# Kernel optimization log

Hardware: AMD Instinct MI355X
Metric: run time of the kernel (lower is better)

The kernel has to match this reference:

```python
import jax, jax.numpy as jnp
import numpy as np
from jax import lax

POOL = 4  # hp['gcn_pool_size']


def sparsemax(z):
    # sparsemax along last axis (Martins & Astudillo 2016), matches tfa.activations.sparsemax
    n = z.shape[-1]
    z_sorted = jnp.flip(jnp.sort(z, axis=-1), axis=-1)          # descending
    k = jnp.arange(1, n + 1, dtype=z.dtype)
    zcum = jnp.cumsum(z_sorted, axis=-1)
    support = (1.0 + k * z_sorted) > zcum                        # [.., n] bool
    k_sel = jnp.sum(support, axis=-1, keepdims=True)             # int, >= 1
    tau = (jnp.take_along_axis(zcum, k_sel - 1, axis=-1) - 1.0) / k_sel.astype(z.dtype)
    return jnp.maximum(z - tau, 0.0)


def gcn_layer(x, W):
    # x: [B, T, E]
    T = x.shape[1]
    # einsum('Bte,bte->tBb') then mean over t == contract over t,e and divide by T
    adj = jnp.einsum('Bte,bte->Bb', x, x) / T                    # [B, B]
    adj = sparsemax(adj)                                         # row-wise sparsemax
    m = adj[:, :, None, None] * x[None]                          # [B, b, T, E] outer product
    # MaxPool2D((POOL,1), stride 1, 'same') on [batch=B, H=b, W=T, C=E]: pool over neighbor axis b
    m = lax.reduce_window(m, -jnp.inf, lax.max,
                          (1, POOL, 1, 1), (1, 1, 1, 1), 'SAME')
    agg = jnp.sum(m, axis=1)                                     # [B, T, E]
    return jax.nn.relu(agg @ W)                                  # [B, T, rel_dim]


def setup_inputs() -> dict:
    key = jax.random.key(0)
    k0, k1, k2, k3 = jax.random.split(key, 4)
    B, T, E = 64, 256, 64
    rel_dim, n_stack = 4, 8
    x = jax.random.normal(k0, (B, T, E), dtype=jnp.float32)
    W0 = jax.random.normal(k1, (E, rel_dim), dtype=jnp.float32) * 0.1
    W1 = jax.random.normal(k2, (rel_dim, rel_dim), dtype=jnp.float32) * 0.1
    Wp = jax.random.normal(k3, (rel_dim, n_stack), dtype=jnp.float32) * 0.1
    return {"x": x, "W0": W0, "W1": W1, "Wp": Wp}


def reference(x, W0, W1, Wp):
    x = gcn_layer(x, W0)           # layer 0: E -> rel_dim
    x = gcn_layer(x, W1)           # layer 1: rel_dim -> rel_dim
    pooled = jnp.mean(x, axis=1)   # [B, rel_dim], mean over T
    return jax.nn.softmax(pooled @ Wp, axis=-1)  # [B, n_stack]
```

## Files before the change

### kernel.cpp

```cpp
#include <hip/hip_runtime.h>
#include <math.h>

__device__ __forceinline__ float4 f4max(float4 a, float4 b) {
    return make_float4(fmaxf(a.x, b.x), fmaxf(a.y, b.y), fmaxf(a.z, b.z), fmaxf(a.w, b.w));
}
__device__ __forceinline__ float4 f4scale(float s, float4 v) {
    return make_float4(s * v.x, s * v.y, s * v.z, s * v.w);
}
__device__ __forceinline__ float4 f4add(float4 a, float4 b) {
    return make_float4(a.x + b.x, a.y + b.y, a.z + b.z, a.w + b.w);
}
__device__ __forceinline__ float4 f4fma(float a, float4 b, float4 c) {
    return make_float4(fmaf(a, b.x, c.x), fmaf(a, b.y, c.y), fmaf(a, b.z, c.z), fmaf(a, b.w, c.w));
}
__device__ __forceinline__ float4 f4fma4(float4 a, float4 b, float4 c) {
    return make_float4(fmaf(a.x, b.x, c.x), fmaf(a.y, b.y, c.y),
                       fmaf(a.z, b.z, c.z), fmaf(a.w, b.w, c.w));
}

__device__ __forceinline__ void store_f4_llc(float* p, float4 v) {
    __hip_atomic_store(p + 0, v.x, __ATOMIC_RELAXED, __HIP_MEMORY_SCOPE_AGENT);
    __hip_atomic_store(p + 1, v.y, __ATOMIC_RELAXED, __HIP_MEMORY_SCOPE_AGENT);
    __hip_atomic_store(p + 2, v.z, __ATOMIC_RELAXED, __HIP_MEMORY_SCOPE_AGENT);
    __hip_atomic_store(p + 3, v.w, __ATOMIC_RELAXED, __HIP_MEMORY_SCOPE_AGENT);
}

__device__ __forceinline__ float wave_sparsemax(float z, int lane) {
    float v = z;
    for (int k = 2; k <= 64; k <<= 1) {
        bool desc = (lane & k) == 0;
        for (int j = k >> 1; j > 0; j >>= 1) {
            float other = __shfl_xor(v, j, 64);
            bool lower = (lane & j) == 0;
            float mn = fminf(v, other), mx = fmaxf(v, other);
            v = (desc ^ lower) ? mn : mx;
        }
    }
    float c = v;
    for (int d = 1; d < 64; d <<= 1) {
        float n = __shfl_up(c, d, 64);
        if (lane >= d) c += n;
    }
    bool sup = (1.0f + (float)(lane + 1) * v) > c;
    int ksel = __popcll(__ballot(sup));
    float zk = __shfl(c, ksel - 1, 64);
    float tau = (zk - 1.0f) / (float)ksel;
    return fmaxf(z - tau, 0.f);
}

__device__ unsigned g_grp[16 * 64];
__device__ unsigned g_glb;
__device__ unsigned g_gen1;
__device__ unsigned g_gen2;

__device__ __forceinline__ void sync_point(int bx, unsigned snap, unsigned* genp,
                                           bool wait) {
    __syncthreads();
    if (threadIdx.x == 0) {
        unsigned a = __hip_atomic_fetch_add(&g_grp[(bx & 15) << 6], 1u,
                                            __ATOMIC_RELAXED, __HIP_MEMORY_SCOPE_AGENT);
        if ((a & 15u) == 15u) {
            unsigned ga = __hip_atomic_fetch_add(&g_glb, 1u, __ATOMIC_RELAXED,
                                                 __HIP_MEMORY_SCOPE_AGENT);
            if ((ga & 15u) == 15u)
                __hip_atomic_fetch_add(genp, 1u, __ATOMIC_RELAXED,
                                       __HIP_MEMORY_SCOPE_AGENT);
        }
        if (wait) {
            while (__hip_atomic_load(genp, __ATOMIC_RELAXED,
                                     __HIP_MEMORY_SCOPE_AGENT) == snap)
                __builtin_amdgcn_s_sleep(1);
            __builtin_amdgcn_fence(__ATOMIC_ACQUIRE, "agent");
        }
    }
    if (wait) __syncthreads();
}

__global__ __launch_bounds__(256)
void fused_gcn(const float* __restrict__ x, const float* __restrict__ W0,
               const float* __restrict__ W1, const float* __restrict__ Wp,
               float* __restrict__ P, float* __restrict__ h0,
               float* __restrict__ out) {
    __shared__ float xsT[64][68];
    __shared__ float pstg[4][4][64];
    __shared__ float psm_s[4][64];
    __shared__ __align__(16) float row[4 * 260];
    __shared__ float part[256];
    __shared__ float psmD[64];
    __shared__ float red[16];

    int tid = threadIdx.x;
    int bx = blockIdx.x;
    int lane = tid & 63;

    unsigned snap1 = 0, snap2 = 0;
    if (tid == 0) {
        snap1 = __hip_atomic_load(&g_gen1, __ATOMIC_RELAXED, __HIP_MEMORY_SCOPE_AGENT);
        snap2 = __hip_atomic_load(&g_gen2, __ATOMIC_RELAXED, __HIP_MEMORY_SCOPE_AGENT);
    }

    {
        int k0 = bx * 64;
#pragma unroll
        for (int it = 0; it < 4; ++it) {
            int f = it * 256 + tid;
            int i = f >> 4, k4 = (f & 15) * 4;
            float4 v = *(const float4*)(x + (size_t)i * 16384 + k0 + k4);
            xsT[k4 + 0][i] = v.x; xsT[k4 + 1][i] = v.y;
            xsT[k4 + 2][i] = v.z; xsT[k4 + 3][i] = v.w;
        }
        __syncthreads();
        int ti = (tid >> 4) * 4, tj = (tid & 15) * 4;
        float4 a0 = make_float4(0, 0, 0, 0), a1 = a0, a2 = a0, a3 = a0;
#pragma unroll 8
        for (int k = 0; k < 64; ++k) {
            float4 a = *(const float4*)&xsT[k][ti];
            float4 b = *(const float4*)&xsT[k][tj];
            a0 = f4fma(a.x, b, a0); a1 = f4fma(a.y, b, a1);
            a2 = f4fma(a.z, b, a2); a3 = f4fma(a.w, b, a3);
        }
        float* basep = P + ((size_t)bx << 12);
        store_f4_llc(basep + (ti + 0) * 64 + tj, a0);
        store_f4_llc(basep + (ti + 1) * 64 + tj, a1);
        store_f4_llc(basep + (ti + 2) * 64 + tj, a2);
        store_f4_llc(basep + (ti + 3) * 64 + tj, a3);
    }
    sync_point(bx, snap1, &g_gen1, true);

    {
        int w4 = tid >> 6;
        int Bc = (bx & 15) * 4;
        int rowi = Bc + w4;
        int sub = (tid & 63) >> 4;
        int c16 = tid & 15;
        const float* pb = P + (size_t)rowi * 64 + c16 * 4;
        float4 g = make_float4(0, 0, 0, 0);
        int cbase = sub * 64;
#pragma unroll 8
        for (int i = 0; i < 64; ++i)
            g = f4add(g, *(const float4*)(pb + ((size_t)(cbase + i) << 12)));
        *(float4*)&pstg[w4][sub][c16 * 4] = g;
        __syncthreads();
        {
            float z = (((pstg[w4][0][lane] + pstg[w4][1][lane])
                        + pstg[w4][2][lane]) + pstg[w4][3][lane]) * (1.0f / 256.0f);
            psm_s[w4][lane] = wave_sparsemax(z, lane);
        }
        __syncthreads();
    }

    {
        int t0 = (bx >> 4) * 16;
        int Bc = (bx & 15) * 4;
        int w = __builtin_amdgcn_readfirstlane(tid >> 6);
        int tq = lane >> 4, eq = lane & 15;
        int t = t0 + (w << 2) + tq;
        float4 w0r0 = *(const float4*)(W0 + (eq * 4 + 0) * 4);
        float4 w0r1 = *(const float4*)(W0 + (eq * 4 + 1) * 4);
        float4 w0r2 = *(const float4*)(W0 + (eq * 4 + 2) * 4);
        float4 w0r3 = *(const float4*)(W0 + (eq * 4 + 3) * 4);
        const float4* xg = (const float4*)(x + ((size_t)t * 64) + eq * 4);
        float4 qm1[4], qb[4], vt[4], acc[4];
        float4 xA = xg[0];
        float4 xB = xg[4096];
#pragma unroll
        for (int h = 0; h < 4; ++h) {
            float4 v = f4scale(psm_s[h][0], xA);
            vt[h] = f4scale(psm_s[h][1], xB);
            qm1[h] = v;
            qb[h] = f4max(v, vt[h]);
            acc[h] = make_float4(0, 0, 0, 0);
        }
#pragma unroll 4
        for (int bl = 0; bl < 62; ++bl) {
            float4 xn = xg[(size_t)(bl + 2) * 4096];
#pragma unroll
            for (int h = 0; h < 4; ++h) {
                float4 vn = f4scale(psm_s[h][bl + 2], xn);
                float4 q1 = f4max(vt[h], vn);
                acc[h] = f4add(acc[h], f4max(qm1[h], q1));
                qm1[h] = qb[h]; qb[h] = q1; vt[h] = vn;
            }
        }
#pragma unroll
        for (int h = 0; h < 4; ++h) {
            acc[h] = f4add(acc[h], f4max(qm1[h], vt[h]));
            acc[h] = f4add(acc[h], qb[h]);
            float4 a = acc[h];
            float4 hh = f4fma(a.x, w0r0, f4fma(a.y, w0r1,
                       f4fma(a.z, w0r2, f4scale(a.w, w0r3))));
            for (int m = 1; m <= 8; m <<= 1) {
                hh.x += __shfl_xor(hh.x, m, 64);
                hh.y += __shfl_xor(hh.y, m, 64);
                hh.z += __shfl_xor(hh.z, m, 64);
                hh.w += __shfl_xor(hh.w, m, 64);
            }
            if (eq == 0) {
                int B = Bc + h;
                float4 r = make_float4(fmaxf(hh.x, 0.f), fmaxf(hh.y, 0.f),
                                       fmaxf(hh.z, 0.f), fmaxf(hh.w, 0.f));
                store_f4_llc(h0 + (size_t)(B * 256 + t) * 4, r);
            }
        }
    }
    sync_point(bx, snap2, &g_gen2, bx < 64);

    if (bx < 64) {
        int bid = bx;
        {
            int q = tid >> 6, s2 = (tid & 63) * 4;
            *(float4*)(row + q * 260 + s2) = *(const float4*)(h0 + (size_t)bid * 1024 + tid * 4);
        }
        __syncthreads();
        {
            int j = tid >> 2, q = tid & 3;
            const float4* hj = (const float4*)(h0 + (size_t)j * 1024 + q * 256);
            const float4* ri = (const float4*)(row + q * 260);
            float4 s4 = make_float4(0, 0, 0, 0);
#pragma unroll 8
            for (int kk = 0; kk < 64; ++kk) s4 = f4fma4(ri[kk], hj[kk], s4);
            part[tid] = s4.x + s4.y + s4.z + s4.w;
        }
        __syncthreads();
        if (tid < 64) {
            float z = (part[lane * 4] + part[lane * 4 + 1] + part[lane * 4 + 2]
                       + part[lane * 4 + 3]) * (1.0f / 256.0f);
            psmD[lane] = wave_sparsemax(z, lane);
        }
        __syncthreads();
        int w = __builtin_amdgcn_readfirstlane(tid >> 6);
        int rc = lane & 3;
        float psum = 0.f;
#pragma unroll
        for (int gg = 0; gg < 4; ++gg) {
            int tbase = w * 64 + gg * 16;
            const float* xb = h0 + (size_t)tbase * 4 + lane;
            float v0 = psmD[0] * xb[0];
            float v1 = psmD[1] * xb[1024];
            float qm1s = v0, qbs = fmaxf(v0, v1), vts = v1, accs = 0.f;
#pragma unroll 8
            for (int bl = 0; bl < 62; ++bl) {
                float vn = psmD[bl + 2] * xb[(size_t)(bl + 2) * 1024];
                float q1 = fmaxf(vts, vn);
                accs += fmaxf(qm1s, q1);
                qm1s = qbs; qbs = q1; vts = vn;
            }
            accs += fmaxf(qm1s, vts);
            accs += qbs;
            int base = lane & ~3;
            float b0 = __shfl(accs, base + 0, 64);
            float b1 = __shfl(accs, base + 1, 64);
            float b2 = __shfl(accs, base + 2, 64);
            float b3 = __shfl(accs, base + 3, 64);
            float h = b0 * W1[rc] + b1 * W1[4 + rc] + b2 * W1[8 + rc] + b3 * W1[12 + rc];
            psum += fmaxf(h, 0.f);
        }
        for (int m = 4; m <= 32; m <<= 1) psum += __shfl_xor(psum, m, 64);
        if (lane < 4) red[w * 4 + lane] = psum;
        __syncthreads();
        if (tid < 64) {
            float pooled = 0.f;
            if (lane < 4)
                pooled = (red[lane] + red[4 + lane] + red[8 + lane] + red[12 + lane])
                         * (1.0f / 256.0f);
            float q0 = __shfl(pooled, 0, 64), q1 = __shfl(pooled, 1, 64);
            float q2 = __shfl(pooled, 2, 64), q3 = __shfl(pooled, 3, 64);
            float logit = -INFINITY;
            if (lane < 8)
                logit = q0 * Wp[lane] + q1 * Wp[8 + lane]
                      + q2 * Wp[16 + lane] + q3 * Wp[24 + lane];
            float mx = logit;
            for (int m = 4; m >= 1; m >>= 1) mx = fmaxf(mx, __shfl_xor(mx, m, 8));
            float e = (lane < 8) ? __expf(logit - mx) : 0.f;
            float s = e;
            for (int m = 4; m >= 1; m >>= 1) s += __shfl_xor(s, m, 8);
            if (lane < 8) out[bid * 8 + lane] = e / s;
        }
    }
}

extern "C" void kernel_launch(void* const* d_in, const int* in_sizes, int n_in,
                              void* d_out, int out_size, void* d_ws, size_t ws_size,
                              hipStream_t stream) {
    const float* x  = (const float*)d_in[0];
    const float* W0 = (const float*)d_in[1];
    const float* W1 = (const float*)d_in[2];
    const float* Wp = (const float*)d_in[3];
    float* out = (float*)d_out;

    char* ws = (char*)d_ws;
    float* P  = (float*)ws;
    float* h0 = (float*)(ws + (4u << 20));

    fused_gcn<<<256, 256, 0, stream>>>(x, W0, W1, Wp, P, h0, out);
}
```

Before: 116.5 us.

## Deduplicate cross-block partial reduction via extra grid barrier and staging buffer

Replaces the per-block redundant reduction of Gram-matrix partials (each of 16 blocks per row group re-reading all 256 partial chunks) with a one-time distributed reduction into a new P2 staging buffer. This is followed by an additional grid-wide sync before blocks read their reduced rows. It aims to cut L2/global read traffic by a factor of 16, at the cost of a third grid barrier and a reduction phase where only 4 lanes per wave are active.

```diff
diff --git a/kernel.cpp b/kernel.cpp
--- a/kernel.cpp
+++ b/kernel.cpp
@@ -51,6 +51,7 @@
 __device__ unsigned g_grp[16 * 64];
 __device__ unsigned g_glb;
 __device__ unsigned g_gen1;
+__device__ unsigned g_gen3;
 __device__ unsigned g_gen2;
 
 __device__ __forceinline__ void sync_point(int bx, unsigned snap, unsigned* genp,
@@ -79,8 +80,8 @@
 __global__ __launch_bounds__(256)
 void fused_gcn(const float* __restrict__ x, const float* __restrict__ W0,
                const float* __restrict__ W1, const float* __restrict__ Wp,
-               float* __restrict__ P, float* __restrict__ h0,
-               float* __restrict__ out) {
+               float* __restrict__ P, float* __restrict__ P2,
+               float* __restrict__ h0, float* __restrict__ out) {
     __shared__ float xsT[64][68];
     __shared__ float pstg[4][4][64];
     __shared__ float psm_s[4][64];
@@ -93,10 +94,11 @@
     int bx = blockIdx.x;
     int lane = tid & 63;
 
-    unsigned snap1 = 0, snap2 = 0;
+    unsigned snap1 = 0, snap2 = 0, snap3 = 0;
     if (tid == 0) {
         snap1 = __hip_atomic_load(&g_gen1, __ATOMIC_RELAXED, __HIP_MEMORY_SCOPE_AGENT);
-        snap2 = __hip_atomic_load(&g_gen2, __ATOMIC_RELAXED, __HIP_MEMORY_SCOPE_AGENT);
+        snap2 = __hip_atomic_load(&g_gen3, __ATOMIC_RELAXED, __HIP_MEMORY_SCOPE_AGENT);
+        snap3 = __hip_atomic_load(&g_gen2, __ATOMIC_RELAXED, __HIP_MEMORY_SCOPE_AGENT);
     }
 
     {
@@ -129,17 +131,30 @@
 
     {
         int w4 = tid >> 6;
+        int l = tid & 63;
+        if (l < 4) {
+            int cid = (bx << 4) + (w4 << 2) + l;
+            int i = cid >> 6;
+            int q = (cid >> 2) & 15;
+            int s = cid & 3;
+            const float* pb = P + (size_t)i * 64 + q * 4;
+            int cbase = s << 6;
+            float4 g = make_float4(0, 0, 0, 0);
+#pragma unroll 8
+            for (int c = 0; c < 64; ++c)
+                g = f4add(g, *(const float4*)(pb + ((size_t)(cbase + c) << 12)));
+            store_f4_llc(P2 + (((size_t)(i * 16 + q) * 4 + s) << 2), g);
+        }
+    }
+    sync_point(bx, snap2, &g_gen3, true);
+
+    {
+        int w4 = tid >> 6;
         int Bc = (bx & 15) * 4;
         int rowi = Bc + w4;
-        int sub = (tid & 63) >> 4;
-        int c16 = tid & 15;
-        const float* pb = P + (size_t)rowi * 64 + c16 * 4;
-        float4 g = make_float4(0, 0, 0, 0);
-        int cbase = sub * 64;
-#pragma unroll 8
-        for (int i = 0; i < 64; ++i)
-            g = f4add(g, *(const float4*)(pb + ((size_t)(cbase + i) << 12)));
-        *(float4*)&pstg[w4][sub][c16 * 4] = g;
+        int q = lane >> 2, s = lane & 3;
+        float4 v = *(const float4*)(P2 + (((size_t)(rowi * 16 + q) * 4 + s) << 2));
+        *(float4*)&pstg[w4][s][q * 4] = v;
         __syncthreads();
         {
             float z = (((pstg[w4][0][lane] + pstg[w4][1][lane])
@@ -203,7 +218,7 @@
             }
         }
     }
-    sync_point(bx, snap2, &g_gen2, bx < 64);
+    sync_point(bx, snap3, &g_gen2, bx < 64);
 
     if (bx < 64) {
         int bid = bx;
@@ -291,6 +306,7 @@
     char* ws = (char*)d_ws;
     float* P  = (float*)ws;
     float* h0 = (float*)(ws + (4u << 20));
-
-    fused_gcn<<<256, 256, 0, stream>>>(x, W0, W1, Wp, P, h0, out);
-}
+    float* P2 = (float*)(ws + (4u << 20) + 262144u);
+
+    fused_gcn<<<256, 256, 0, stream>>>(x, W0, W1, Wp, P, P2, h0, out);
+}
```

Result: slower. 121.9 us (+4.7%).

## Double block size to 512 threads and split per-wave work across more waves

Applied to the files above, without the earlier changes.

Launches 512 threads per block instead of 256. Each phase redistributes its work: the Gram tile computes 2 rows per thread, the aggregation phase gives each wave 2 batch rows instead of 4, and the final layer-1 phase packs two batch items per block using 32 blocks. The aim is to shorten the serial chain per wave and raise latency hiding in the memory-bound streaming loops, at the cost of more barrier participants and idle waves during the sparsemax reduction.

```diff
diff --git a/kernel.cpp b/kernel.cpp
--- a/kernel.cpp
+++ b/kernel.cpp
@@ -76,7 +76,7 @@
     if (wait) __syncthreads();
 }
 
-__global__ __launch_bounds__(256)
+__global__ __launch_bounds__(512)
 void fused_gcn(const float* __restrict__ x, const float* __restrict__ W0,
                const float* __restrict__ W1, const float* __restrict__ Wp,
                float* __restrict__ P, float* __restrict__ h0,
@@ -84,10 +84,10 @@
     __shared__ float xsT[64][68];
     __shared__ float pstg[4][4][64];
     __shared__ float psm_s[4][64];
-    __shared__ __align__(16) float row[4 * 260];
-    __shared__ float part[256];
-    __shared__ float psmD[64];
-    __shared__ float red[16];
+    __shared__ __align__(16) float rowD[2][4 * 260];
+    __shared__ float part[2][256];
+    __shared__ float psmD[2][64];
+    __shared__ float redD[2][16];
 
     int tid = threadIdx.x;
     int bx = blockIdx.x;
@@ -102,57 +102,59 @@
     {
         int k0 = bx * 64;
 #pragma unroll
-        for (int it = 0; it < 4; ++it) {
-            int f = it * 256 + tid;
+        for (int it = 0; it < 2; ++it) {
+            int f = it * 512 + tid;
             int i = f >> 4, k4 = (f & 15) * 4;
             float4 v = *(const float4*)(x + (size_t)i * 16384 + k0 + k4);
             xsT[k4 + 0][i] = v.x; xsT[k4 + 1][i] = v.y;
             xsT[k4 + 2][i] = v.z; xsT[k4 + 3][i] = v.w;
         }
         __syncthreads();
-        int ti = (tid >> 4) * 4, tj = (tid & 15) * 4;
-        float4 a0 = make_float4(0, 0, 0, 0), a1 = a0, a2 = a0, a3 = a0;
+        int ti = (tid >> 4) * 2, tj = (tid & 15) * 4;
+        float4 a0 = make_float4(0, 0, 0, 0), a1 = a0;
 #pragma unroll 8
         for (int k = 0; k < 64; ++k) {
-            float4 a = *(const float4*)&xsT[k][ti];
+            float ax = xsT[k][ti], ay = xsT[k][ti + 1];
             float4 b = *(const float4*)&xsT[k][tj];
-            a0 = f4fma(a.x, b, a0); a1 = f4fma(a.y, b, a1);
-            a2 = f4fma(a.z, b, a2); a3 = f4fma(a.w, b, a3);
+            a0 = f4fma(ax, b, a0); a1 = f4fma(ay, b, a1);
         }
         float* basep = P + ((size_t)bx << 12);
         store_f4_llc(basep + (ti + 0) * 64 + tj, a0);
         store_f4_llc(basep + (ti + 1) * 64 + tj, a1);
-        store_f4_llc(basep + (ti + 2) * 64 + tj, a2);
-        store_f4_llc(basep + (ti + 3) * 64 + tj, a3);
     }
     sync_point(bx, snap1, &g_gen1, true);
 
     {
-        int w4 = tid >> 6;
+        int w8 = tid >> 6;
         int Bc = (bx & 15) * 4;
-        int rowi = Bc + w4;
-        int sub = (tid & 63) >> 4;
-        int c16 = tid & 15;
-        const float* pb = P + (size_t)rowi * 64 + c16 * 4;
-        float4 g = make_float4(0, 0, 0, 0);
-        int cbase = sub * 64;
+        if (w8 < 4) {
+            int rowi = Bc + w8;
+            int sub = lane >> 4;
+            int c16 = lane & 15;
+            const float* pb = P + (size_t)rowi * 64 + c16 * 4;
+            int cbase = sub * 64;
+            float4 g = make_float4(0, 0, 0, 0);
 #pragma unroll 8
-        for (int i = 0; i < 64; ++i)
-            g = f4add(g, *(const float4*)(pb + ((size_t)(cbase + i) << 12)));
-        *(float4*)&pstg[w4][sub][c16 * 4] = g;
-        __syncthreads();
-        {
-            float z = (((pstg[w4][0][lane] + pstg[w4][1][lane])
-                        + pstg[w4][2][lane]) + pstg[w4][3][lane]) * (1.0f / 256.0f);
-            psm_s[w4][lane] = wave_sparsemax(z, lane);
+            for (int c = 0; c < 64; ++c)
+                g = f4add(g, *(const float4*)(pb + ((size_t)(cbase + c) << 12)));
+            *(float4*)&pstg[w8][sub][c16 * 4] = g;
+        }
+        __syncthreads();
+        if (w8 < 4) {
+            float z = (((pstg[w8][0][lane] + pstg[w8][1][lane])
+                        + pstg[w8][2][lane]) + pstg[w8][3][lane]) * (1.0f / 256.0f);
+            psm_s[w8][lane] = wave_sparsemax(z, lane);
         }
         __syncthreads();
     }
 
     {
         int t0 = (bx >> 4) * 16;
-        int Bc = (bx & 15) * 4;
-        int w = __builtin_amdgcn_readfirstlane(tid >> 6);
+        int BcBase = (bx & 15) * 4;
+        int w8 = __builtin_amdgcn_readfirstlane(tid >> 6);
+        int vb = w8 >> 2;
+        int w = w8 & 3;
+        int hb = vb * 2;
         int tq = lane >> 4, eq = lane & 15;
         int t = t0 + (w << 2) + tq;
         float4 w0r0 = *(const float4*)(W0 + (eq * 4 + 0) * 4);
@@ -160,13 +162,13 @@
         float4 w0r2 = *(const float4*)(W0 + (eq * 4 + 2) * 4);
         float4 w0r3 = *(const float4*)(W0 + (eq * 4 + 3) * 4);
         const float4* xg = (const float4*)(x + ((size_t)t * 64) + eq * 4);
-        float4 qm1[4], qb[4], vt[4], acc[4];
+        float4 qm1[2], qb[2], vt[2], acc[2];
         float4 xA = xg[0];
         float4 xB = xg[4096];
 #pragma unroll
-        for (int h = 0; h < 4; ++h) {
-            float4 v = f4scale(psm_s[h][0], xA);
-            vt[h] = f4scale(psm_s[h][1], xB);
+        for (int h = 0; h < 2; ++h) {
+            float4 v = f4scale(psm_s[hb + h][0], xA);
+            vt[h] = f4scale(psm_s[hb + h][1], xB);
             qm1[h] = v;
             qb[h] = f4max(v, vt[h]);
             acc[h] = make_float4(0, 0, 0, 0);
@@ -175,15 +177,15 @@
         for (int bl = 0; bl < 62; ++bl) {
             float4 xn = xg[(size_t)(bl + 2) * 4096];
 #pragma unroll
-            for (int h = 0; h < 4; ++h) {
-                float4 vn = f4scale(psm_s[h][bl + 2], xn);
+            for (int h = 0; h < 2; ++h) {
+                float4 vn = f4scale(psm_s[hb + h][bl + 2], xn);
                 float4 q1 = f4max(vt[h], vn);
                 acc[h] = f4add(acc[h], f4max(qm1[h], q1));
                 qm1[h] = qb[h]; qb[h] = q1; vt[h] = vn;
             }
         }
 #pragma unroll
-        for (int h = 0; h < 4; ++h) {
+        for (int h = 0; h < 2; ++h) {
             acc[h] = f4add(acc[h], f4max(qm1[h], vt[h]));
             acc[h] = f4add(acc[h], qb[h]);
             float4 a = acc[h];
@@ -196,51 +198,55 @@
                 hh.w += __shfl_xor(hh.w, m, 64);
             }
             if (eq == 0) {
-                int B = Bc + h;
+                int B = BcBase + hb + h;
                 float4 r = make_float4(fmaxf(hh.x, 0.f), fmaxf(hh.y, 0.f),
                                        fmaxf(hh.z, 0.f), fmaxf(hh.w, 0.f));
                 store_f4_llc(h0 + (size_t)(B * 256 + t) * 4, r);
             }
         }
     }
-    sync_point(bx, snap2, &g_gen2, bx < 64);
-
-    if (bx < 64) {
-        int bid = bx;
+    sync_point(bx, snap2, &g_gen2, bx < 32);
+
+    if (bx < 32) {
+        int vb = tid >> 8;
+        int ttid = tid & 255;
+        int bid = bx * 2 + vb;
         {
-            int q = tid >> 6, s2 = (tid & 63) * 4;
-            *(float4*)(row + q * 260 + s2) = *(const float4*)(h0 + (size_t)bid * 1024 + tid * 4);
+            int q = ttid >> 6, s2 = lane * 4;
+            *(float4*)(rowD[vb] + q * 260 + s2) =
+                *(const float4*)(h0 + (size_t)bid * 1024 + ttid * 4);
         }
         __syncthreads();
         {
-            int j = tid >> 2, q = tid & 3;
+            int j = ttid >> 2, q = ttid & 3;
             const float4* hj = (const float4*)(h0 + (size_t)j * 1024 + q * 256);
-            const float4* ri = (const float4*)(row + q * 260);
+            const float4* ri = (const float4*)(rowD[vb] + q * 260);
             float4 s4 = make_float4(0, 0, 0, 0);
 #pragma unroll 8
             for (int kk = 0; kk < 64; ++kk) s4 = f4fma4(ri[kk], hj[kk], s4);
-            part[tid] = s4.x + s4.y + s4.z + s4.w;
-        }
-        __syncthreads();
-        if (tid < 64) {
-            float z = (part[lane * 4] + part[lane * 4 + 1] + part[lane * 4 + 2]
-                       + part[lane * 4 + 3]) * (1.0f / 256.0f);
-            psmD[lane] = wave_sparsemax(z, lane);
-        }
-        __syncthreads();
-        int w = __builtin_amdgcn_readfirstlane(tid >> 6);
+            part[vb][ttid] = s4.x + s4.y + s4.z + s4.w;
+        }
+        __syncthreads();
+        if (ttid < 64) {
+            float z = (part[vb][lane * 4] + part[vb][lane * 4 + 1]
+                       + part[vb][lane * 4 + 2] + part[vb][lane * 4 + 3])
+                      * (1.0f / 256.0f);
+            psmD[vb][lane] = wave_sparsemax(z, lane);
+        }
+        __syncthreads();
+        int w = __builtin_amdgcn_readfirstlane((tid >> 6) & 3);
         int rc = lane & 3;
         float psum = 0.f;
 #pragma unroll
         for (int gg = 0; gg < 4; ++gg) {
             int tbase = w * 64 + gg * 16;
             const float* xb = h0 + (size_t)tbase * 4 + lane;
-            float v0 = psmD[0] * xb[0];
-            float v1 = psmD[1] * xb[1024];
+            float v0 = psmD[vb][0] * xb[0];
+            float v1 = psmD[vb][1] * xb[1024];
             float qm1s = v0, qbs = fmaxf(v0, v1), vts = v1, accs = 0.f;
 #pragma unroll 8
             for (int bl = 0; bl < 62; ++bl) {
-                float vn = psmD[bl + 2] * xb[(size_t)(bl + 2) * 1024];
+                float vn = psmD[vb][bl + 2] * xb[(size_t)(bl + 2) * 1024];
                 float q1 = fmaxf(vts, vn);
                 accs += fmaxf(qm1s, q1);
                 qm1s = qbs; qbs = q1; vts = vn;
@@ -256,13 +262,13 @@
             psum += fmaxf(h, 0.f);
         }
         for (int m = 4; m <= 32; m <<= 1) psum += __shfl_xor(psum, m, 64);
-        if (lane < 4) red[w * 4 + lane] = psum;
-        __syncthreads();
-        if (tid < 64) {
+        if (lane < 4) redD[vb][w * 4 + lane] = psum;
+        __syncthreads();
+        if (ttid < 64) {
             float pooled = 0.f;
             if (lane < 4)
-                pooled = (red[lane] + red[4 + lane] + red[8 + lane] + red[12 + lane])
-                         * (1.0f / 256.0f);
+                pooled = (redD[vb][lane] + redD[vb][4 + lane] + redD[vb][8 + lane]
+                          + redD[vb][12 + lane]) * (1.0f / 256.0f);
             float q0 = __shfl(pooled, 0, 64), q1 = __shfl(pooled, 1, 64);
             float q2 = __shfl(pooled, 2, 64), q3 = __shfl(pooled, 3, 64);
             float logit = -INFINITY;
@@ -292,5 +298,5 @@
     float* P  = (float*)ws;
     float* h0 = (float*)(ws + (4u << 20));
 
-    fused_gcn<<<256, 256, 0, stream>>>(x, W0, W1, Wp, P, h0, out);
-}
+    fused_gcn<<<256, 512, 0, stream>>>(x, W0, W1, Wp, P, h0, out);
+}
```

Result: slower. 119.0 us (+2.2%).
